# Performance work log

Hardware: AMD Instinct MI355X
Metric: run time of the kernel (lower is better)

Reference implementation:

```python
import jax, jax.numpy as jnp
import numpy as np
import math

N = 20000      # nodes
E = 320000     # edges
D = 256        # in_dim == out_dim (residual requires equality)
H = 8          # heads
K = D // H     # k_dim = 32
T = 3          # node types
R = 5          # edge (relation) types
C = 16         # output classes
SQRT_K = math.sqrt(K)


def setup_inputs() -> dict:
    key = jax.random.key(0)
    ks = jax.random.split(key, 18)
    x = jax.random.normal(ks[0], (N, D), jnp.float32)
    edge_index = jax.random.randint(ks[1], (2, E), 0, N, jnp.int32)
    node_type = jax.random.randint(ks[2], (N,), 0, T, jnp.int32)
    edge_type = jax.random.randint(ks[3], (E,), 0, R, jnp.int32)
    g_lin = math.sqrt(2.0 / (D + D))
    g_rel = math.sqrt(2.0 / (K + K))
    g_out = math.sqrt(2.0 / (D + C))
    Wk = jax.random.normal(ks[4], (T, D, D), jnp.float32) * g_lin
    bk = jnp.zeros((T, D), jnp.float32)
    Wq = jax.random.normal(ks[5], (T, D, D), jnp.float32) * g_lin
    bq = jnp.zeros((T, D), jnp.float32)
    Wv = jax.random.normal(ks[6], (T, D, D), jnp.float32) * g_lin
    bv = jnp.zeros((T, D), jnp.float32)
    Wa = jax.random.normal(ks[7], (T, D, D), jnp.float32) * g_lin
    ba = jnp.zeros((T, D), jnp.float32)
    rel_prior = jnp.ones((R, H), jnp.float32)
    rel_att = jax.random.normal(ks[8], (R, H, K, K), jnp.float32) * g_rel
    rel_msg = jax.random.normal(ks[9], (R, H, K, K), jnp.float32) * g_rel
    W_out = jax.random.normal(ks[10], (D, C), jnp.float32) * g_out
    b_out = jnp.zeros((C,), jnp.float32)
    return {"x": x, "edge_index": edge_index, "node_type": node_type,
            "edge_type": edge_type, "Wk": Wk, "bk": bk, "Wq": Wq, "bq": bq,
            "Wv": Wv, "bv": bv, "Wa": Wa, "ba": ba, "rel_prior": rel_prior,
            "rel_att": rel_att, "rel_msg": rel_msg, "W_out": W_out, "b_out": b_out}


def _typed_linear(h, W, b, node_type):
    # per-node-type Linear: small fixed loop over T types, masked select
    out = jnp.zeros((h.shape[0], W.shape[2]), h.dtype)
    for t in range(T):
        m = (node_type == t)[:, None]
        out = out + jnp.where(m, h @ W[t] + b[t], 0.0)
    return out


def _hgt_forward(x, edge_index, node_type, edge_type, Wk, bk, Wq, bq, Wv, bv,
                 Wa, ba, rel_prior, rel_att, rel_msg, W_out, b_out):
    src, dst = edge_index[0], edge_index[1]
    # typed projections -> [N, H, K]
    Kn = _typed_linear(x, Wk, bk, node_type).reshape(N, H, K)
    Qn = _typed_linear(x, Wq, bq, node_type).reshape(N, H, K)
    Vn = _typed_linear(x, Wv, bv, node_type).reshape(N, H, K)
    Ke, Qe, Ve = Kn[src], Qn[dst], Vn[src]  # [E, H, K] gathers
    # relation-specific bilinear transforms of K and V (fixed loop over R)
    Kt = jnp.zeros_like(Ke)
    Mt = jnp.zeros_like(Ve)
    for r in range(R):
        m = (edge_type == r)[:, None, None]
        Kt = Kt + jnp.where(m, jnp.einsum('ehk,hkl->ehl', Ke, rel_att[r]), 0.0)
        Mt = Mt + jnp.where(m, jnp.einsum('ehk,hkl->ehl', Ve, rel_msg[r]), 0.0)
    # attention logits with relation prior, scaled by sqrt(k_dim)
    logits = (Qe * Kt).sum(-1) * rel_prior[edge_type] / SQRT_K  # [E, H]
    # segment softmax over incoming edges per destination node
    mx = jax.ops.segment_max(logits, dst, num_segments=N)       # [N, H]
    ex = jnp.exp(logits - mx[dst])
    sm = jax.ops.segment_sum(ex, dst, num_segments=N)           # [N, H]
    att = ex / sm[dst]                                          # [E, H]
    # weighted messages, scatter-add aggregation
    msg = (Mt * att[:, :, None]).reshape(E, D)
    aggr = jax.ops.segment_sum(msg, dst, num_segments=N)        # [N, D]
    # update: ELU, typed output linear, residual
    h = jax.nn.elu(aggr)
    h = _typed_linear(h, Wa, ba, node_type) + x
    # final classifier + log_softmax
    return jax.nn.log_softmax(h @ W_out + b_out, axis=1)


def reference(x, edge_index, node_type, edge_type, Wk, bk, Wq, bq, Wv, bv,
              Wa, ba, rel_prior, rel_att, rel_msg, W_out, b_out):
    return _hgt_forward(x, edge_index, node_type, edge_type, Wk, bk, Wq, bq,
                        Wv, bv, Wa, ba, rel_prior, rel_att, rel_msg, W_out, b_out)
```

## Files before the change

kernel.cpp:

```cpp
#include <hip/hip_runtime.h>
#include <hip/hip_bf16.h>
#include <math.h>

#define NN 20000
#define NE 320000
#define DD 256
#define NH 8
#define KK 32
#define NR 5
#define NC 16
#define NB2 391

typedef unsigned short u16;
typedef unsigned int u32;
typedef __attribute__((ext_vector_type(8))) short bf16x8;
typedef __attribute__((ext_vector_type(4))) float f32x4;

__device__ __forceinline__ float bf2f(u16 v){ return __uint_as_float(((u32)v)<<16); }
__device__ __forceinline__ u16 f2bf(float f){
  u32 u = __float_as_uint(f);
  return (u16)((u + 0x7FFFu + ((u>>16)&1u)) >> 16);
}

__global__ void k_nb_count(const int* __restrict__ ntype, int* __restrict__ cnt){
  int n = blockIdx.x*256 + threadIdx.x;
  int t = (n < NN) ? ntype[n] : -1;
  int lane = threadIdx.x & 63;
  #pragma unroll
  for(int tt=0; tt<3; tt++){
    unsigned long long mask = __ballot(t == tt);
    int leader = __ffsll((long long)mask) - 1;
    if(lane == leader) atomicAdd(&cnt[tt], __popcll(mask));
  }
}
__global__ void k_nb_off(const int* __restrict__ cnt, int* __restrict__ boff){
  int a = (cnt[0]+31)&~31;
  int b = (cnt[1]+31)&~31;
  boff[0]=0; boff[1]=a; boff[2]=a+b;
}
__global__ void k_nb_scatter(const int* __restrict__ ntype, const int* __restrict__ boff,
                             int* __restrict__ bcur, int* __restrict__ perm){
  int n = blockIdx.x*256 + threadIdx.x;
  int t = (n < NN) ? ntype[n] : -1;
  int lane = threadIdx.x & 63;
  #pragma unroll
  for(int tt=0; tt<3; tt++){
    unsigned long long mask = __ballot(t == tt);
    if(t == tt){
      int rank = __popcll(mask & ((1ull<<lane)-1ull));
      int leader = __ffsll((long long)mask) - 1;
      int base = 0;
      if(lane == leader) base = atomicAdd(&bcur[tt], __popcll(mask));
      base = __shfl(base, leader);
      perm[boff[tt] + base + rank] = n;
    }
  }
}

__global__ void k_deg(const int* __restrict__ ei, const int* __restrict__ etype,
                      int* __restrict__ off2){
  int e = blockIdx.x*256 + threadIdx.x;
  if(e < NE) atomicAdd(&off2[ei[NE + e]*NR + etype[e]], 1);
}
__global__ __launch_bounds__(256) void k_scan1(int* __restrict__ off2, int* __restrict__ bsum){
  __shared__ int sh[256];
  int t = threadIdx.x;
  int i = blockIdx.x*256 + t;
  int v = (i < NN*NR) ? off2[i] : 0;
  sh[t] = v;
  __syncthreads();
  for(int off=1; off<256; off<<=1){
    int val = (t >= off) ? sh[t-off] : 0;
    __syncthreads();
    sh[t] += val;
    __syncthreads();
  }
  if(i < NN*NR) off2[i] = sh[t] - v;
  if(t == 255) bsum[blockIdx.x] = sh[255];
}
__global__ __launch_bounds__(512) void k_scan2(int* __restrict__ bsum, int* __restrict__ off2){
  __shared__ int sh[512];
  int t = threadIdx.x;
  int v = (t < NB2) ? bsum[t] : 0;
  sh[t] = v;
  __syncthreads();
  for(int off=1; off<512; off<<=1){
    int val = (t >= off) ? sh[t-off] : 0;
    __syncthreads();
    sh[t] += val;
    __syncthreads();
  }
  if(t < NB2) bsum[t] = sh[t] - v;
  if(t == 511) off2[NN*NR] = sh[511];
}
__global__ __launch_bounds__(256) void k_scan3(int* __restrict__ off2, const int* __restrict__ bsum){
  int i = blockIdx.x*256 + threadIdx.x;
  if(i < NN*NR) off2[i] += bsum[blockIdx.x];
}
__global__ void k_escatter(const int* __restrict__ ei, const int* __restrict__ etype,
                           int* __restrict__ off2, int* __restrict__ packed){
  int e = blockIdx.x*256 + threadIdx.x;
  if(e < NE){
    int pos = atomicAdd(&off2[ei[NE+e]*NR + etype[e]], 1);
    packed[pos] = ei[e];
  }
}

__global__ void k_castx(const float* __restrict__ x, u16* __restrict__ xb){
  int i = blockIdx.x*256 + threadIdx.x;
  float4 v0 = ((const float4*)x)[i*2+0];
  float4 v1 = ((const float4*)x)[i*2+1];
  uint4 o;
  o.x = (u32)f2bf(v0.x) | ((u32)f2bf(v0.y)<<16);
  o.y = (u32)f2bf(v0.z) | ((u32)f2bf(v0.w)<<16);
  o.z = (u32)f2bf(v1.x) | ((u32)f2bf(v1.y)<<16);
  o.w = (u32)f2bf(v1.z) | ((u32)f2bf(v1.w)<<16);
  ((uint4*)xb)[i] = o;
}

__global__ __launch_bounds__(256) void k_castw(
  const float* __restrict__ Wk, const float* __restrict__ Wq,
  const float* __restrict__ Wv, const float* __restrict__ Wa,
  u16* __restrict__ Wtk, u16* __restrict__ Wtq,
  u16* __restrict__ Wtv, u16* __restrict__ Wta)
{
  __shared__ float tile[32][33];
  int z = blockIdx.z;
  int tensor = z/3, t = z%3;
  const float* W = (tensor==0) ? Wk : (tensor==1) ? Wq : (tensor==2) ? Wv : Wa;
  u16* O = (tensor==0) ? Wtk : (tensor==1) ? Wtq : (tensor==2) ? Wtv : Wta;
  int i0 = blockIdx.x*32, j0 = blockIdx.y*32;
  int rr = threadIdx.x>>5, cc = threadIdx.x&31;
  #pragma unroll
  for(int p=0;p<4;p++)
    tile[rr+p*8][cc] = W[t*65536 + (i0+rr+p*8)*256 + j0+cc];
  __syncthreads();
  #pragma unroll
  for(int p=0;p<4;p++)
    O[t*65536 + (j0+rr+p*8)*256 + i0+cc] = f2bf(tile[cc][rr+p*8]);
}

__global__ void k_castm(const float* __restrict__ rmsg, u16* __restrict__ Mtm){
  int idx = blockIdx.x*256 + threadIdx.x;
  int l = idx & 31, k = (idx >> 5) & 31, rh = idx >> 10;
  Mtm[(rh*32 + l)*32 + k] = f2bf(rmsg[idx]);
}

__global__ void k_casta(const float* __restrict__ ratt, const float* __restrict__ prior,
                        u16* __restrict__ Atb){
  int idx = blockIdx.x*256 + threadIdx.x;
  int rh = idx >> 10;
  float scale = prior[rh] * 0.17677669529663687f;
  Atb[idx] = f2bf(ratt[idx] * scale);
}

__global__ void k_casto(const float* __restrict__ Wo, u16* __restrict__ Wot){
  int idx = blockIdx.x*256 + threadIdx.x;
  int c = idx & 15, k = idx >> 4;
  Wot[c*DD + k] = f2bf(Wo[k*NC + c]);
}

#define XSP 264
__global__ __launch_bounds__(256) void k_proj(
    const u16* __restrict__ xb, const int* __restrict__ perm, const int* __restrict__ boff,
    const u16* __restrict__ Wtk, const u16* __restrict__ Wtq, const u16* __restrict__ Wtv,
    const float* __restrict__ bk, const float* __restrict__ bq, const float* __restrict__ bv,
    u16* __restrict__ KVn, u16* __restrict__ Qnb)
{
  __shared__ u16 smem[32*XSP];
  __shared__ int gids[32];
  int tid = threadIdx.x;
  int ts = (blockIdx.x >> 1)*32;
  int cb = (blockIdx.x & 1)*128;
  int t = (ts >= boff[2]) ? 2 : (ts >= boff[1]) ? 1 : 0;
  if(tid < 32) gids[tid] = perm[ts + tid];
  __syncthreads();
  #pragma unroll
  for(int it=0; it<4; it++){
    int q = tid + it*256;
    int row = q >> 5, c = q & 31;
    int g = gids[row];
    uint4 v = make_uint4(0,0,0,0);
    if(g >= 0) v = ((const uint4*)(xb + (size_t)g*DD))[c];
    ((uint4*)(smem + row*XSP))[c] = v;
  }
  __syncthreads();
  int lane = tid & 63;
  int w = tid >> 6;
  int quad = lane >> 4;
  int l16 = lane & 15;
  f32x4 accK[2][2], accQ[2][2], accV[2][2];
  #pragma unroll
  for(int mt=0;mt<2;mt++)
    #pragma unroll
    for(int nt=0;nt<2;nt++){
      accK[mt][nt]=(f32x4)(0.f); accQ[mt][nt]=(f32x4)(0.f); accV[mt][nt]=(f32x4)(0.f);
    }
  const u16* wkp = Wtk + (size_t)t*65536;
  const u16* wqp = Wtq + (size_t)t*65536;
  const u16* wvp = Wtv + (size_t)t*65536;
  #pragma unroll
  for(int kk=0; kk<8; kk++){
    int kb = kk*32 + quad*8;
    bf16x8 a0 = *(const bf16x8*)(smem + l16*XSP + kb);
    bf16x8 a1 = *(const bf16x8*)(smem + (16+l16)*XSP + kb);
    #pragma unroll
    for(int nt=0; nt<2; nt++){
      int n = cb + w*32 + nt*16 + l16;
      bf16x8 bK = *(const bf16x8*)(wkp + (size_t)n*DD + kb);
      bf16x8 bQ = *(const bf16x8*)(wqp + (size_t)n*DD + kb);
      bf16x8 bV = *(const bf16x8*)(wvp + (size_t)n*DD + kb);
      accK[0][nt] = __builtin_amdgcn_mfma_f32_16x16x32_bf16(a0, bK, accK[0][nt], 0,0,0);
      accK[1][nt] = __builtin_amdgcn_mfma_f32_16x16x32_bf16(a1, bK, accK[1][nt], 0,0,0);
      accQ[0][nt] = __builtin_amdgcn_mfma_f32_16x16x32_bf16(a0, bQ, accQ[0][nt], 0,0,0);
      accQ[1][nt] = __builtin_amdgcn_mfma_f32_16x16x32_bf16(a1, bQ, accQ[1][nt], 0,0,0);
      accV[0][nt] = __builtin_amdgcn_mfma_f32_16x16x32_bf16(a0, bV, accV[0][nt], 0,0,0);
      accV[1][nt] = __builtin_amdgcn_mfma_f32_16x16x32_bf16(a1, bV, accV[1][nt], 0,0,0);
    }
  }
  __syncthreads();
  #pragma unroll
  for(int nt=0; nt<2; nt++){
    int lc = w*32 + nt*16 + l16;
    int colg = cb + lc;
    int kvo = ((lc >> 2)*8 + (lc & 3));
    float bkv = bk[t*DD+colg], bvv = bv[t*DD+colg];
    #pragma unroll
    for(int mt=0; mt<2; mt++){
      #pragma unroll
      for(int reg=0; reg<4; reg++){
        int row = mt*16 + quad*4 + reg;
        smem[row*XSP + kvo]     = f2bf(accK[mt][nt][reg] + bkv);
        smem[row*XSP + kvo + 4] = f2bf(accV[mt][nt][reg] + bvv);
      }
    }
  }
  __syncthreads();
  #pragma unroll
  for(int it=0; it<4; it++){
    int q = tid + it*256;
    int row = q >> 5, c = q & 31;
    int g = gids[row];
    if(g >= 0)
      *(uint4*)(KVn + (size_t)g*512 + (cb>>2)*8 + c*8) = ((uint4*)(smem + row*XSP))[c];
  }
  __syncthreads();
  #pragma unroll
  for(int nt=0; nt<2; nt++){
    int lc = w*32 + nt*16 + l16;
    float bqv = bq[t*DD + cb + lc];
    #pragma unroll
    for(int mt=0; mt<2; mt++){
      #pragma unroll
      for(int reg=0; reg<4; reg++){
        int row = mt*16 + quad*4 + reg;
        smem[row*XSP + lc] = f2bf(accQ[mt][nt][reg] + bqv);
      }
    }
  }
  __syncthreads();
  #pragma unroll
  for(int it=0; it<2; it++){
    int q = tid + it*256;
    int row = q >> 4, c = q & 15;
    int g = gids[row];
    if(g >= 0)
      *(uint4*)(Qnb + (size_t)g*DD + cb + c*8) = ((uint4*)(smem + row*XSP))[c];
  }
}

#define VSP 264
__global__ __launch_bounds__(256) void k_qa(
    const u16* __restrict__ Qnb, const u16* __restrict__ Atb, u16* __restrict__ QA)
{
  __shared__ u16 Vs[32*VSP];
  __shared__ u16 Os[32*VSP];
  int tid = threadIdx.x;
  int n0 = blockIdx.x*32;
  int lane = tid & 63;
  int w = tid >> 6;
  int quad = lane >> 4;
  int l16 = lane & 15;
  #pragma unroll
  for(int it=0; it<4; it++){
    int q = tid + it*256;
    int row = q >> 5, c = q & 31;
    ((uint4*)(Vs + row*VSP))[c] = ((const uint4*)(Qnb + (size_t)(n0+row)*DD))[c];
  }
  __syncthreads();
  for(int r=0; r<NR; r++){
    f32x4 acc[2][2][2];
    #pragma unroll
    for(int hh=0;hh<2;hh++)
      #pragma unroll
      for(int mt=0;mt<2;mt++)
        #pragma unroll
        for(int nt=0;nt<2;nt++) acc[hh][mt][nt]=(f32x4)(0.f);
    #pragma unroll
    for(int hh=0; hh<2; hh++){
      int h = w*2 + hh;
      bf16x8 a0 = *(const bf16x8*)(Vs + l16*VSP + h*32 + quad*8);
      bf16x8 a1 = *(const bf16x8*)(Vs + (16+l16)*VSP + h*32 + quad*8);
      const u16* ap = Atb + (size_t)(r*NH + h)*1024;
      bf16x8 b0 = *(const bf16x8*)(ap + l16*32 + quad*8);
      bf16x8 b1 = *(const bf16x8*)(ap + (16+l16)*32 + quad*8);
      acc[hh][0][0] = __builtin_amdgcn_mfma_f32_16x16x32_bf16(a0, b0, acc[hh][0][0], 0,0,0);
      acc[hh][0][1] = __builtin_amdgcn_mfma_f32_16x16x32_bf16(a0, b1, acc[hh][0][1], 0,0,0);
      acc[hh][1][0] = __builtin_amdgcn_mfma_f32_16x16x32_bf16(a1, b0, acc[hh][1][0], 0,0,0);
      acc[hh][1][1] = __builtin_amdgcn_mfma_f32_16x16x32_bf16(a1, b1, acc[hh][1][1], 0,0,0);
    }
    #pragma unroll
    for(int hh=0; hh<2; hh++){
      int h = w*2 + hh;
      #pragma unroll
      for(int mt=0; mt<2; mt++){
        #pragma unroll
        for(int nt=0; nt<2; nt++){
          #pragma unroll
          for(int reg=0; reg<4; reg++){
            int row = mt*16 + quad*4 + reg;
            Os[row*VSP + h*32 + nt*16 + l16] = f2bf(acc[hh][mt][nt][reg]);
          }
        }
      }
    }
    __syncthreads();
    #pragma unroll
    for(int it=0; it<4; it++){
      int q = tid + it*256;
      int row = q >> 5, c = q & 31;
      *(uint4*)(QA + ((size_t)(n0+row)*NR + r)*DD + c*8) = ((uint4*)(Os + row*VSP))[c];
    }
    __syncthreads();
  }
}

__global__ __launch_bounds__(256) void k_edge(
    const u16* __restrict__ KVn, const u16* __restrict__ QA,
    const int* __restrict__ off2, const int* __restrict__ packed,
    u16* __restrict__ aggrV)
{
  int lane = threadIdx.x & 63;
  int n = blockIdx.x*4 + (threadIdx.x >> 6);
  if(n >= NN) return;
  int off = lane*4;
  float4 qa[NR];
  {
    const u16* qp = QA + (size_t)n*NR*DD + off;
    #pragma unroll
    for(int r=0;r<NR;r++){
      ushort4 q = *(const ushort4*)(qp + r*DD);
      qa[r] = make_float4(bf2f(q.x),bf2f(q.y),bf2f(q.z),bf2f(q.w));
    }
  }
  int eb[NR+1];
  eb[0] = (n==0) ? 0 : off2[n*NR - 1];
  #pragma unroll
  for(int i=1;i<=NR;i++) eb[i] = off2[n*NR + i - 1];
  float4 acc[NR];
  float s = 0.f;
  int lo8 = lane*8;

  #define EDGE_DOT(kv, q, dd) \
    { float k0=__uint_as_float((kv).x<<16), k1=__uint_as_float((kv).x&0xffff0000u); \
      float k2=__uint_as_float((kv).y<<16), k3=__uint_as_float((kv).y&0xffff0000u); \
      dd = k0*(q).x + k1*(q).y + k2*(q).z + k3*(q).w; }
  #define EDGE_ACC(kv, p, a) \
    { float v0=__uint_as_float((kv).z<<16), v1=__uint_as_float((kv).z&0xffff0000u); \
      float v2=__uint_as_float((kv).w<<16), v3=__uint_as_float((kv).w&0xffff0000u); \
      (a).x += (p)*v0; (a).y += (p)*v1; (a).z += (p)*v2; (a).w += (p)*v3; }
  #define RED3(d) { d += __shfl_xor(d,1); d += __shfl_xor(d,2); d += __shfl_xor(d,4); }

  #pragma unroll
  for(int r=0;r<NR;r++){
    float4 q = qa[r];
    float4 a = make_float4(0.f,0.f,0.f,0.f);
    int e = eb[r], end = eb[r+1];
    for(; e+4 <= end; e += 4){
      int s0 = packed[e], s1 = packed[e+1], s2 = packed[e+2], s3 = packed[e+3];
      uint4 kv0 = *(const uint4*)(KVn + (size_t)s0*512 + lo8);
      uint4 kv1 = *(const uint4*)(KVn + (size_t)s1*512 + lo8);
      uint4 kv2 = *(const uint4*)(KVn + (size_t)s2*512 + lo8);
      uint4 kv3 = *(const uint4*)(KVn + (size_t)s3*512 + lo8);
      float d0,d1,d2,d3;
      EDGE_DOT(kv0,q,d0); EDGE_DOT(kv1,q,d1); EDGE_DOT(kv2,q,d2); EDGE_DOT(kv3,q,d3);
      RED3(d0); RED3(d1); RED3(d2); RED3(d3);
      float p0=__expf(d0), p1=__expf(d1), p2=__expf(d2), p3=__expf(d3);
      s += p0 + p1 + p2 + p3;
      EDGE_ACC(kv0,p0,a); EDGE_ACC(kv1,p1,a); EDGE_ACC(kv2,p2,a); EDGE_ACC(kv3,p3,a);
    }
    if(e+2 <= end){
      int s0 = packed[e], s1 = packed[e+1];
      uint4 kv0 = *(const uint4*)(KVn + (size_t)s0*512 + lo8);
      uint4 kv1 = *(const uint4*)(KVn + (size_t)s1*512 + lo8);
      float d0,d1;
      EDGE_DOT(kv0,q,d0); EDGE_DOT(kv1,q,d1);
      RED3(d0); RED3(d1);
      float p0=__expf(d0), p1=__expf(d1);
      s += p0 + p1;
      EDGE_ACC(kv0,p0,a); EDGE_ACC(kv1,p1,a);
      e += 2;
    }
    if(e < end){
      int s0 = packed[e];
      uint4 kv0 = *(const uint4*)(KVn + (size_t)s0*512 + lo8);
      float d0;
      EDGE_DOT(kv0,q,d0);
      RED3(d0);
      float p0=__expf(d0);
      s += p0;
      EDGE_ACC(kv0,p0,a);
    }
    acc[r] = a;
  }
  #undef EDGE_DOT
  #undef EDGE_ACC
  #undef RED3
  float inv = (s > 0.f) ? (1.f/s) : 0.f;
  u16* op = aggrV + (size_t)n*NR*DD + off;
  #pragma unroll
  for(int r=0;r<NR;r++){
    ushort4 o;
    o.x=f2bf(acc[r].x*inv); o.y=f2bf(acc[r].y*inv);
    o.z=f2bf(acc[r].z*inv); o.w=f2bf(acc[r].w*inv);
    *(ushort4*)(op + r*DD) = o;
  }
}

__global__ __launch_bounds__(256) void k_msg(
    const u16* __restrict__ aggrV, const u16* __restrict__ Mtm,
    u16* __restrict__ h1b)
{
  __shared__ u16 Vs[32*VSP];
  int tid = threadIdx.x;
  int n0 = blockIdx.x*32;
  int lane = tid & 63;
  int w = tid >> 6;
  int quad = lane >> 4;
  int l16 = lane & 15;
  f32x4 acc[2][2][2];
  #pragma unroll
  for(int hh=0;hh<2;hh++)
    #pragma unroll
    for(int mt=0;mt<2;mt++)
      #pragma unroll
      for(int nt=0;nt<2;nt++) acc[hh][mt][nt]=(f32x4)(0.f);
  for(int r=0;r<NR;r++){
    __syncthreads();
    #pragma unroll
    for(int it=0; it<4; it++){
      int q = tid + it*256;
      int row = q >> 5, c = q & 31;
      ((uint4*)(Vs + row*VSP))[c] =
        ((const uint4*)(aggrV + ((size_t)(n0+row)*NR + r)*DD))[c];
    }
    __syncthreads();
    #pragma unroll
    for(int hh=0; hh<2; hh++){
      int h = w*2 + hh;
      bf16x8 a0 = *(const bf16x8*)(Vs + l16*VSP + h*32 + quad*8);
      bf16x8 a1 = *(const bf16x8*)(Vs + (16+l16)*VSP + h*32 + quad*8);
      const u16* mp = Mtm + ((size_t)(r*NH + h)*32)*32;
      bf16x8 b0 = *(const bf16x8*)(mp + l16*32 + quad*8);
      bf16x8 b1 = *(const bf16x8*)(mp + (16+l16)*32 + quad*8);
      acc[hh][0][0] = __builtin_amdgcn_mfma_f32_16x16x32_bf16(a0, b0, acc[hh][0][0], 0,0,0);
      acc[hh][0][1] = __builtin_amdgcn_mfma_f32_16x16x32_bf16(a0, b1, acc[hh][0][1], 0,0,0);
      acc[hh][1][0] = __builtin_amdgcn_mfma_f32_16x16x32_bf16(a1, b0, acc[hh][1][0], 0,0,0);
      acc[hh][1][1] = __builtin_amdgcn_mfma_f32_16x16x32_bf16(a1, b1, acc[hh][1][1], 0,0,0);
    }
  }
  #pragma unroll
  for(int hh=0; hh<2; hh++){
    int h = w*2 + hh;
    #pragma unroll
    for(int mt=0; mt<2; mt++){
      #pragma unroll
      for(int nt=0; nt<2; nt++){
        #pragma unroll
        for(int reg=0; reg<4; reg++){
          int n = n0 + mt*16 + quad*4 + reg;
          float v = acc[hh][mt][nt][reg];
          v = (v > 0.f) ? v : expm1f(v);
          h1b[(size_t)n*DD + h*32 + nt*16 + l16] = f2bf(v);
        }
      }
    }
  }
}

__global__ __launch_bounds__(256) void k_out(
    const u16* __restrict__ h1b, const float* __restrict__ x,
    const int* __restrict__ perm, const int* __restrict__ boff,
    const u16* __restrict__ Wta, const float* __restrict__ ba,
    const u16* __restrict__ Wot, const float* __restrict__ bo,
    float* __restrict__ out)
{
  __shared__ u16 hs[32*VSP];
  __shared__ u16 h2s[32*VSP];
  __shared__ int gids[32];
  int tid = threadIdx.x;
  int ts = blockIdx.x*32;
  int t = (ts >= boff[2]) ? 2 : (ts >= boff[1]) ? 1 : 0;
  if(tid < 32) gids[tid] = perm[ts + tid];
  __syncthreads();
  #pragma unroll
  for(int it=0; it<4; it++){
    int q = tid + it*256;
    int row = q >> 5, c = q & 31;
    int g = gids[row];
    uint4 v = make_uint4(0,0,0,0);
    if(g >= 0) v = ((const uint4*)(h1b + (size_t)g*DD))[c];
    ((uint4*)(hs + row*VSP))[c] = v;
  }
  __syncthreads();
  int lane = tid & 63, w = tid >> 6, quad = lane >> 4, l16 = lane & 15;
  f32x4 acc[2][4];
  #pragma unroll
  for(int mt=0;mt<2;mt++)
    #pragma unroll
    for(int nt=0;nt<4;nt++) acc[mt][nt]=(f32x4)(0.f);
  const u16* wap = Wta + (size_t)t*65536;
  #pragma unroll
  for(int kk=0; kk<8; kk++){
    int kb = kk*32 + quad*8;
    bf16x8 a0 = *(const bf16x8*)(hs + l16*VSP + kb);
    bf16x8 a1 = *(const bf16x8*)(hs + (16+l16)*VSP + kb);
    #pragma unroll
    for(int nt=0; nt<4; nt++){
      int n = w*64 + nt*16 + l16;
      bf16x8 b = *(const bf16x8*)(wap + (size_t)n*DD + kb);
      acc[0][nt] = __builtin_amdgcn_mfma_f32_16x16x32_bf16(a0, b, acc[0][nt], 0,0,0);
      acc[1][nt] = __builtin_amdgcn_mfma_f32_16x16x32_bf16(a1, b, acc[1][nt], 0,0,0);
    }
  }
  #pragma unroll
  for(int nt=0; nt<4; nt++){
    int colg = w*64 + nt*16 + l16;
    float bav = ba[t*DD + colg];
    #pragma unroll
    for(int mt=0; mt<2; mt++){
      #pragma unroll
      for(int reg=0; reg<4; reg++){
        int row = mt*16 + quad*4 + reg;
        int g = gids[row];
        float xr = (g>=0) ? x[(size_t)g*DD + colg] : 0.f;
        h2s[row*VSP + colg] = f2bf(acc[mt][nt][reg] + bav + xr);
      }
    }
  }
  __syncthreads();
  if(w < 2){
    f32x4 cacc = (f32x4)(0.f);
    #pragma unroll
    for(int kk=0; kk<8; kk++){
      int kb = kk*32 + quad*8;
      bf16x8 a = *(const bf16x8*)(h2s + (w*16 + l16)*VSP + kb);
      bf16x8 b = *(const bf16x8*)(Wot + (size_t)l16*DD + kb);
      cacc = __builtin_amdgcn_mfma_f32_16x16x32_bf16(a, b, cacc, 0,0,0);
    }
    float bov = bo[l16];
    #pragma unroll
    for(int reg=0; reg<4; reg++){
      int row = w*16 + quad*4 + reg;
      int g = gids[row];
      float v = cacc[reg] + bov;
      float m = v;
      m = fmaxf(m, __shfl_xor(m,1)); m = fmaxf(m, __shfl_xor(m,2));
      m = fmaxf(m, __shfl_xor(m,4)); m = fmaxf(m, __shfl_xor(m,8));
      float p = __expf(v - m);
      p += __shfl_xor(p,1); p += __shfl_xor(p,2);
      p += __shfl_xor(p,4); p += __shfl_xor(p,8);
      float lse = m + __logf(p);
      if(g >= 0) out[(size_t)g*NC + l16] = v - lse;
    }
  }
}

extern "C" void kernel_launch(void* const* d_in, const int* in_sizes, int n_in,
                              void* d_out, int out_size, void* d_ws, size_t ws_size,
                              hipStream_t stream)
{
  const float* x     = (const float*)d_in[0];
  const int*   ei    = (const int*)d_in[1];
  const int*   ntype = (const int*)d_in[2];
  const int*   etype = (const int*)d_in[3];
  const float* Wk    = (const float*)d_in[4];
  const float* bk    = (const float*)d_in[5];
  const float* Wq    = (const float*)d_in[6];
  const float* bq    = (const float*)d_in[7];
  const float* Wv    = (const float*)d_in[8];
  const float* bv    = (const float*)d_in[9];
  const float* Wa    = (const float*)d_in[10];
  const float* ba    = (const float*)d_in[11];
  const float* prior = (const float*)d_in[12];
  const float* ratt  = (const float*)d_in[13];
  const float* rmsg  = (const float*)d_in[14];
  const float* Wo    = (const float*)d_in[15];
  const float* bo    = (const float*)d_in[16];
  float* out = (float*)d_out;

  char* ws = (char*)d_ws;
  int* iw      = (int*)ws;
  int* cnt     = iw + 0;
  int* bcur    = iw + 4;
  int* boff    = iw + 8;
  int* off2    = iw + 16;
  int* perm    = iw + 100032;
  int* packed  = iw + 120128;
  int* bsum    = iw + 440128;

  size_t fb = 1762560;
  u16*   Qnb   = (u16*)(ws + fb);   fb += 4ull*NN*DD;
  char*  h1reg = (char*)(ws + fb);  fb += 4ull*NN*DD;
  u16*   KVn   = (u16*)(ws + fb);   fb += 4ull*NN*DD;
  u16*   QA    = (u16*)(ws + fb);   fb += 2ull*NN*NR*DD;
  u16*   aggrV = (u16*)(ws + fb);   fb += 2ull*NN*NR*DD;
  u16* Wtk = (u16*)h1reg;
  u16* Wtq = Wtk + 3*65536;
  u16* Wtv = Wtq + 3*65536;
  u16* h1b = (u16*)h1reg;
  u16* Wta = (u16*)(h1reg + 11534336);
  u16* Wot = Wta + 3*65536;
  u16* Mtm = (u16*)(h1reg + 12582912);
  u16* Atb = (u16*)(h1reg + 13631488);
  u16* xb  = aggrV;

  hipMemsetAsync(iw, 0, (size_t)(16 + NN*NR + 1)*sizeof(int), stream);
  hipMemsetAsync(perm, 0xFF, (size_t)20096*sizeof(int), stream);

  k_nb_count  <<<79, 256, 0, stream>>>(ntype, cnt);
  k_nb_off    <<<1, 1, 0, stream>>>(cnt, boff);
  k_nb_scatter<<<79, 256, 0, stream>>>(ntype, boff, bcur, perm);
  k_deg       <<<1250, 256, 0, stream>>>(ei, etype, off2);
  k_scan1     <<<NB2, 256, 0, stream>>>(off2, bsum);
  k_scan2     <<<1, 512, 0, stream>>>(bsum, off2);
  k_scan3     <<<NB2, 256, 0, stream>>>(off2, bsum);
  k_escatter  <<<1250, 256, 0, stream>>>(ei, etype, off2, packed);
  k_castm     <<<160, 256, 0, stream>>>(rmsg, Mtm);
  k_casta     <<<160, 256, 0, stream>>>(ratt, prior, Atb);
  k_castx     <<<2500, 256, 0, stream>>>(x, xb);
  k_castw     <<<dim3(8,8,12), 256, 0, stream>>>(Wk, Wq, Wv, Wa, Wtk, Wtq, Wtv, Wta);
  k_casto     <<<16, 256, 0, stream>>>(Wo, Wot);
  k_proj      <<<1256, 256, 0, stream>>>(xb, perm, boff, Wtk, Wtq, Wtv, bk, bq, bv, KVn, Qnb);
  k_qa        <<<625, 256, 0, stream>>>(Qnb, Atb, QA);
  k_edge      <<<5000, 256, 0, stream>>>(KVn, QA, off2, packed, aggrV);
  k_msg       <<<625, 256, 0, stream>>>(aggrV, Mtm, h1b);
  k_out       <<<628, 256, 0, stream>>>(h1b, x, perm, boff, Wta, ba, Wot, bo, out);
}
```

Baseline: 327.9 us.

## Fuse message transform into typed output kernel and merge small cast kernels

The per-relation message MFMA and ELU (k_msg) are merged into the typed output linear kernel (k_out). Each block now gathers aggrV rows by the type-sorted permutation and keeps the ELU result in shared memory, so the h1b round trip through global memory and one launch go away. The three small weight-cast kernels are also merged into a single launch. In exchange, aggrV reads become permuted gathers rather than contiguous loads, and the extra shared buffer may lower occupancy.

```diff
diff --git a/kernel.cpp b/kernel.cpp
--- a/kernel.cpp
+++ b/kernel.cpp
@@ -140,24 +140,25 @@
     O[t*65536 + (j0+rr+p*8)*256 + i0+cc] = f2bf(tile[cc][rr+p*8]);
 }
 
-__global__ void k_castm(const float* __restrict__ rmsg, u16* __restrict__ Mtm){
-  int idx = blockIdx.x*256 + threadIdx.x;
-  int l = idx & 31, k = (idx >> 5) & 31, rh = idx >> 10;
-  Mtm[(rh*32 + l)*32 + k] = f2bf(rmsg[idx]);
-}
-
-__global__ void k_casta(const float* __restrict__ ratt, const float* __restrict__ prior,
-                        u16* __restrict__ Atb){
-  int idx = blockIdx.x*256 + threadIdx.x;
-  int rh = idx >> 10;
-  float scale = prior[rh] * 0.17677669529663687f;
-  Atb[idx] = f2bf(ratt[idx] * scale);
-}
-
-__global__ void k_casto(const float* __restrict__ Wo, u16* __restrict__ Wot){
-  int idx = blockIdx.x*256 + threadIdx.x;
-  int c = idx & 15, k = idx >> 4;
-  Wot[c*DD + k] = f2bf(Wo[k*NC + c]);
+__global__ void k_castsmall(const float* __restrict__ rmsg, const float* __restrict__ ratt,
+                            const float* __restrict__ prior, const float* __restrict__ Wo,
+                            u16* __restrict__ Mtm, u16* __restrict__ Atb,
+                            u16* __restrict__ Wot){
+  int b = blockIdx.x;
+  if(b < 160){
+    int idx = b*256 + threadIdx.x;
+    int l = idx & 31, k = (idx >> 5) & 31, rh = idx >> 10;
+    Mtm[(rh*32 + l)*32 + k] = f2bf(rmsg[idx]);
+  } else if(b < 320){
+    int idx = (b-160)*256 + threadIdx.x;
+    int rh = idx >> 10;
+    float scale = prior[rh] * 0.17677669529663687f;
+    Atb[idx] = f2bf(ratt[idx] * scale);
+  } else {
+    int idx = (b-320)*256 + threadIdx.x;
+    int c = idx & 15, k = idx >> 4;
+    Wot[c*DD + k] = f2bf(Wo[k*NC + c]);
+  }
 }
 
 #define XSP 264
@@ -427,32 +428,42 @@
   }
 }
 
-__global__ __launch_bounds__(256) void k_msg(
+__global__ __launch_bounds__(256) void k_mo(
     const u16* __restrict__ aggrV, const u16* __restrict__ Mtm,
-    u16* __restrict__ h1b)
+    const float* __restrict__ x,
+    const int* __restrict__ perm, const int* __restrict__ boff,
+    const u16* __restrict__ Wta, const float* __restrict__ ba,
+    const u16* __restrict__ Wot, const float* __restrict__ bo,
+    float* __restrict__ out)
 {
   __shared__ u16 Vs[32*VSP];
+  __shared__ u16 hs[32*VSP];
+  __shared__ u16 h2s[32*VSP];
+  __shared__ int gids[32];
   int tid = threadIdx.x;
-  int n0 = blockIdx.x*32;
-  int lane = tid & 63;
-  int w = tid >> 6;
-  int quad = lane >> 4;
-  int l16 = lane & 15;
-  f32x4 acc[2][2][2];
+  int ts = blockIdx.x*32;
+  int t = (ts >= boff[2]) ? 2 : (ts >= boff[1]) ? 1 : 0;
+  if(tid < 32) gids[tid] = perm[ts + tid];
+  __syncthreads();
+  int lane = tid & 63, w = tid >> 6, quad = lane >> 4, l16 = lane & 15;
+
+  f32x4 macc[2][2][2];
   #pragma unroll
   for(int hh=0;hh<2;hh++)
     #pragma unroll
     for(int mt=0;mt<2;mt++)
       #pragma unroll
-      for(int nt=0;nt<2;nt++) acc[hh][mt][nt]=(f32x4)(0.f);
+      for(int nt=0;nt<2;nt++) macc[hh][mt][nt]=(f32x4)(0.f);
   for(int r=0;r<NR;r++){
     __syncthreads();
     #pragma unroll
     for(int it=0; it<4; it++){
       int q = tid + it*256;
       int row = q >> 5, c = q & 31;
-      ((uint4*)(Vs + row*VSP))[c] =
-        ((const uint4*)(aggrV + ((size_t)(n0+row)*NR + r)*DD))[c];
+      int g = gids[row];
+      uint4 v = make_uint4(0,0,0,0);
+      if(g >= 0) v = ((const uint4*)(aggrV + ((size_t)g*NR + r)*DD))[c];
+      ((uint4*)(Vs + row*VSP))[c] = v;
     }
     __syncthreads();
     #pragma unroll
@@ -463,10 +474,10 @@
       const u16* mp = Mtm + ((size_t)(r*NH + h)*32)*32;
       bf16x8 b0 = *(const bf16x8*)(mp + l16*32 + quad*8);
       bf16x8 b1 = *(const bf16x8*)(mp + (16+l16)*32 + quad*8);
-      acc[hh][0][0] = __builtin_amdgcn_mfma_f32_16x16x32_bf16(a0, b0, acc[hh][0][0], 0,0,0);
-      acc[hh][0][1] = __builtin_amdgcn_mfma_f32_16x16x32_bf16(a0, b1, acc[hh][0][1], 0,0,0);
-      acc[hh][1][0] = __builtin_amdgcn_mfma_f32_16x16x32_bf16(a1, b0, acc[hh][1][0], 0,0,0);
-      acc[hh][1][1] = __builtin_amdgcn_mfma_f32_16x16x32_bf16(a1, b1, acc[hh][1][1], 0,0,0);
+      macc[hh][0][0] = __builtin_amdgcn_mfma_f32_16x16x32_bf16(a0, b0, macc[hh][0][0], 0,0,0);
+      macc[hh][0][1] = __builtin_amdgcn_mfma_f32_16x16x32_bf16(a0, b1, macc[hh][0][1], 0,0,0);
+      macc[hh][1][0] = __builtin_amdgcn_mfma_f32_16x16x32_bf16(a1, b0, macc[hh][1][0], 0,0,0);
+      macc[hh][1][1] = __builtin_amdgcn_mfma_f32_16x16x32_bf16(a1, b1, macc[hh][1][1], 0,0,0);
     }
   }
   #pragma unroll
@@ -478,42 +489,16 @@
       for(int nt=0; nt<2; nt++){
         #pragma unroll
         for(int reg=0; reg<4; reg++){
-          int n = n0 + mt*16 + quad*4 + reg;
-          float v = acc[hh][mt][nt][reg];
+          int row = mt*16 + quad*4 + reg;
+          float v = macc[hh][mt][nt][reg];
           v = (v > 0.f) ? v : expm1f(v);
-          h1b[(size_t)n*DD + h*32 + nt*16 + l16] = f2bf(v);
+          hs[row*VSP + h*32 + nt*16 + l16] = f2bf(v);
         }
       }
     }
   }
-}
-
-__global__ __launch_bounds__(256) void k_out(
-    const u16* __restrict__ h1b, const float* __restrict__ x,
-    const int* __restrict__ perm, const int* __restrict__ boff,
-    const u16* __restrict__ Wta, const float* __restrict__ ba,
-    const u16* __restrict__ Wot, const float* __restrict__ bo,
-    float* __restrict__ out)
-{
-  __shared__ u16 hs[32*VSP];
-  __shared__ u16 h2s[32*VSP];
-  __shared__ int gids[32];
-  int tid = threadIdx.x;
-  int ts = blockIdx.x*32;
-  int t = (ts >= boff[2]) ? 2 : (ts >= boff[1]) ? 1 : 0;
-  if(tid < 32) gids[tid] = perm[ts + tid];
-  __syncthreads();
-  #pragma unroll
-  for(int it=0; it<4; it++){
-    int q = tid + it*256;
-    int row = q >> 5, c = q & 31;
-    int g = gids[row];
-    uint4 v = make_uint4(0,0,0,0);
-    if(g >= 0) v = ((const uint4*)(h1b + (size_t)g*DD))[c];
-    ((uint4*)(hs + row*VSP))[c] = v;
-  }
-  __syncthreads();
-  int lane = tid & 63, w = tid >> 6, quad = lane >> 4, l16 = lane & 15;
+  __syncthreads();
+
   f32x4 acc[2][4];
   #pragma unroll
   for(int mt=0;mt<2;mt++)
@@ -618,7 +603,6 @@
   u16* Wtk = (u16*)h1reg;
   u16* Wtq = Wtk + 3*65536;
   u16* Wtv = Wtq + 3*65536;
-  u16* h1b = (u16*)h1reg;
   u16* Wta = (u16*)(h1reg + 11534336);
   u16* Wot = Wta + 3*65536;
   u16* Mtm = (u16*)(h1reg + 12582912);
@@ -636,14 +620,11 @@
   k_scan2     <<<1, 512, 0, stream>>>(bsum, off2);
   k_scan3     <<<NB2, 256, 0, stream>>>(off2, bsum);
   k_escatter  <<<1250, 256, 0, stream>>>(ei, etype, off2, packed);
-  k_castm     <<<160, 256, 0, stream>>>(rmsg, Mtm);
-  k_casta     <<<160, 256, 0, stream>>>(ratt, prior, Atb);
+  k_castsmall <<<336, 256, 0, stream>>>(rmsg, ratt, prior, Wo, Mtm, Atb, Wot);
   k_castx     <<<2500, 256, 0, stream>>>(x, xb);
   k_castw     <<<dim3(8,8,12), 256, 0, stream>>>(Wk, Wq, Wv, Wa, Wtk, Wtq, Wtv, Wta);
-  k_casto     <<<16, 256, 0, stream>>>(Wo, Wot);
   k_proj      <<<1256, 256, 0, stream>>>(xb, perm, boff, Wtk, Wtq, Wtv, bk, bq, bv, KVn, Qnb);
   k_qa        <<<625, 256, 0, stream>>>(Qnb, Atb, QA);
   k_edge      <<<5000, 256, 0, stream>>>(KVn, QA, off2, packed, aggrV);
-  k_msg       <<<625, 256, 0, stream>>>(aggrV, Mtm, h1b);
-  k_out       <<<628, 256, 0, stream>>>(h1b, x, perm, boff, Wta, ba, Wot, bo, out);
-}
+  k_mo        <<<628, 256, 0, stream>>>(aggrV, Mtm, x, perm, boff, Wta, ba, Wot, bo, out);
+}
```

Result: faster. 320.1 us (-2.4%).
